# Kernel tuning notes

Measured on AMD Instinct MI355X. Metric: run time of the kernel, lower is better.

The kernel has to match this reference:

```python
import jax, jax.numpy as jnp
import numpy as np

SIGMA = 0.05
SIGMA2 = SIGMA * SIGMA
N_NODES = 100000
N_EDGES = 3200000


def setup_inputs() -> dict:
    key = jax.random.key(0)
    k1, k2, k3, k4 = jax.random.split(key, 4)
    source_points = jax.random.normal(k1, (N_NODES, 3), dtype=jnp.float32)
    target_points = jax.random.normal(k2, (N_NODES, 3), dtype=jnp.float32)
    edge_index = jax.random.randint(k3, (2, N_EDGES), 0, N_NODES, dtype=jnp.int64)
    edge_weights = jax.random.uniform(k4, (N_EDGES, 1), dtype=jnp.float32)
    return {"source_points": source_points, "target_points": target_points,
            "edge_index": edge_index, "edge_weights": edge_weights}


def reference(source_points, target_points, edge_index, edge_weights):
    N = source_points.shape[0]
    dst = edge_index[0]  # center point each edge contributes to
    nbr = edge_index[1]  # neighbor point index

    src_nb = source_points[nbr]            # [E,3]
    tgt_nb = target_points[nbr]            # [E,3]

    ones_e = jnp.ones((edge_index.shape[1],), dtype=source_points.dtype)
    counts = jnp.maximum(jax.ops.segment_sum(ones_e, dst, num_segments=N), 1.0)[:, None]
    src_centers = jax.ops.segment_sum(src_nb, dst, num_segments=N) / counts  # [N,3]
    tgt_centers = jax.ops.segment_sum(tgt_nb, dst, num_segments=N) / counts  # [N,3]

    src_diff = (src_nb - src_centers[dst]) * edge_weights  # [E,3]
    tgt_diff = tgt_nb - tgt_centers[dst]                   # [E,3]

    # per-edge outer product, scattered to per-point 3x3 covariances
    edge_mats = src_diff[:, :, None] * tgt_diff[:, None, :]          # [E,3,3]
    point_mats = jax.ops.segment_sum(edge_mats, dst, num_segments=N)  # [N,3,3]

    U, S, Vh = jnp.linalg.svd(point_mats)  # torch.svd's V = Vh^T, so U @ V^T == U @ Vh
    R0 = jnp.matmul(U, Vh)
    det = jnp.linalg.det(R0)
    ones_n = jnp.ones((N,), dtype=source_points.dtype)
    d_diag = jax.lax.stop_gradient(jnp.stack([ones_n, ones_n, det], axis=-1))  # [N,3]
    R = jnp.matmul(U * d_diag[:, None, :], Vh)  # U @ diag(d) @ Vh, proper rotation

    trans = tgt_centers - jnp.einsum('nij,nj->ni', R, src_centers)  # [N,3]

    # apply each neighbor's rigid transform and compute robust weights
    transformed = jnp.einsum('eij,ej->ei', R[nbr], src_nb) + trans[nbr]  # [E,3]
    d2 = jnp.sum(jnp.square(transformed - tgt_nb), axis=-1, keepdims=True)  # [E,1]
    new_edge_weights = SIGMA2 / (d2 + SIGMA2)
    return (R, trans, new_edge_weights)
```

## Files before the change

### kernel.cpp

```cpp
#include <hip/hip_runtime.h>
#include <math.h>

static constexpr float kSigma2 = 0.05f * 0.05f;
static constexpr int kCap = 6400;

__device__ __forceinline__ int load_idx(const void* ei, long long j, int is64) {
    if (is64) return (int)(((const long long*)ei)[j]);
    return ((const int*)ei)[j];
}

__global__ void k_detect(const int* __restrict__ ei32, int E, int* __restrict__ nz) {
    int t = threadIdx.x;
    int lim = E < 2048 ? E : 2048;
    int acc = 0;
    for (int k = t; k < lim; k += blockDim.x) acc |= ei32[2 * k + 1];
    if (acc) atomicOr(nz, 1);
}

__global__ void k_pack(const float* __restrict__ src, const float* __restrict__ tgt,
                       float4* __restrict__ s4, float4* __restrict__ t4, int N) {
    int i = blockIdx.x * blockDim.x + threadIdx.x;
    if (i >= N) return;
    s4[i] = make_float4(src[3 * i + 0], src[3 * i + 1], src[3 * i + 2], 0.0f);
    t4[i] = make_float4(tgt[3 * i + 0], tgt[3 * i + 1], tgt[3 * i + 2], 0.0f);
}

__device__ void kabsch_from_M(const double M[3][3], double Rm[3][3]) {
    Rm[0][0] = 1; Rm[0][1] = 0; Rm[0][2] = 0;
    Rm[1][0] = 0; Rm[1][1] = 1; Rm[1][2] = 0;
    Rm[2][0] = 0; Rm[2][1] = 0; Rm[2][2] = 1;

    double frob2 = 0.0;
#pragma unroll
    for (int r = 0; r < 3; ++r)
#pragma unroll
        for (int c = 0; c < 3; ++c) frob2 += M[r][c] * M[r][c];
    if (frob2 <= 1e-80) return;

    double A[3][3];
#pragma unroll
    for (int r = 0; r < 3; ++r)
#pragma unroll
        for (int c = 0; c < 3; ++c) {
            double s = 0.0;
#pragma unroll
            for (int k = 0; k < 3; ++k) s += M[k][r] * M[k][c];
            A[r][c] = s;
        }
    double V[3][3] = {{1, 0, 0}, {0, 1, 0}, {0, 0, 1}};
    const int PL[3] = {0, 0, 1};
    const int QL[3] = {1, 2, 2};
    for (int sweep = 0; sweep < 15; ++sweep) {
        double off = fabs(A[0][1]) + fabs(A[0][2]) + fabs(A[1][2]);
        if (off == 0.0) break;
        for (int pi = 0; pi < 3; ++pi) {
            int p = PL[pi], q = QL[pi], r3 = 3 - p - q;
            double apq = A[p][q];
            if (apq == 0.0) continue;
            double theta = (A[q][q] - A[p][p]) / (2.0 * apq);
            double t = copysign(1.0, theta) / (fabs(theta) + sqrt(theta * theta + 1.0));
            double c = 1.0 / sqrt(t * t + 1.0);
            double s = t * c;
            A[p][p] -= t * apq;
            A[q][q] += t * apq;
            A[p][q] = 0.0; A[q][p] = 0.0;
            double arp = A[r3][p], arq = A[r3][q];
            A[r3][p] = c * arp - s * arq; A[p][r3] = A[r3][p];
            A[r3][q] = s * arp + c * arq; A[q][r3] = A[r3][q];
#pragma unroll
            for (int k = 0; k < 3; ++k) {
                double vp = V[k][p], vq = V[k][q];
                V[k][p] = c * vp - s * vq;
                V[k][q] = s * vp + c * vq;
            }
        }
    }
    double lam[3] = {A[0][0], A[1][1], A[2][2]};
    int id0 = 0, id1 = 1, id2 = 2, tt;
    if (lam[id0] < lam[id1]) { tt = id0; id0 = id1; id1 = tt; }
    if (lam[id0] < lam[id2]) { tt = id0; id0 = id2; id2 = tt; }
    if (lam[id1] < lam[id2]) { tt = id1; id1 = id2; id2 = tt; }
    double v1[3] = {V[0][id0], V[1][id0], V[2][id0]};
    double v2[3] = {V[0][id1], V[1][id1], V[2][id1]};
    double v3[3] = {V[0][id2], V[1][id2], V[2][id2]};

    double b1[3], b2[3];
#pragma unroll
    for (int r = 0; r < 3; ++r) {
        b1[r] = M[r][0] * v1[0] + M[r][1] * v1[1] + M[r][2] * v1[2];
        b2[r] = M[r][0] * v2[0] + M[r][1] * v2[1] + M[r][2] * v2[2];
    }
    double n1 = sqrt(b1[0] * b1[0] + b1[1] * b1[1] + b1[2] * b1[2]);
    if (n1 <= 1e-150) return;
    double u1[3] = {b1[0] / n1, b1[1] / n1, b1[2] / n1};
    double dot = u1[0] * b2[0] + u1[1] * b2[1] + u1[2] * b2[2];
    double w2[3] = {b2[0] - dot * u1[0], b2[1] - dot * u1[1], b2[2] - dot * u1[2]};
    double n2 = sqrt(w2[0] * w2[0] + w2[1] * w2[1] + w2[2] * w2[2]);
    double u2[3];
    if (n2 > n1 * 1e-12) {
        u2[0] = w2[0] / n2; u2[1] = w2[1] / n2; u2[2] = w2[2] / n2;
    } else {
        double ex0 = (fabs(u1[0]) < 0.9) ? 1.0 : 0.0;
        double ex1 = 1.0 - ex0;
        double cx = u1[1] * 0.0 - u1[2] * ex1;
        double cy = u1[2] * ex0 - u1[0] * 0.0;
        double cz = u1[0] * ex1 - u1[1] * ex0;
        double cn = sqrt(cx * cx + cy * cy + cz * cz);
        u2[0] = cx / cn; u2[1] = cy / cn; u2[2] = cz / cn;
    }
    double u3[3] = {u1[1] * u2[2] - u1[2] * u2[1],
                    u1[2] * u2[0] - u1[0] * u2[2],
                    u1[0] * u2[1] - u1[1] * u2[0]};
    double dV = v1[0] * (v2[1] * v3[2] - v2[2] * v3[1])
              - v1[1] * (v2[0] * v3[2] - v2[2] * v3[0])
              + v1[2] * (v2[0] * v3[1] - v2[1] * v3[0]);
    dV = (dV >= 0.0) ? 1.0 : -1.0;
#pragma unroll
    for (int r = 0; r < 3; ++r)
#pragma unroll
        for (int c = 0; c < 3; ++c)
            Rm[r][c] = u1[r] * v1[c] + u2[r] * v2[c] + dV * u3[r] * v3[c];
}


__global__ void __launch_bounds__(256) k_bhist(const void* __restrict__ ei,
                                               int* __restrict__ btot16,
                                               const int* __restrict__ nz,
                                               int E, int N, int nbuckets) {
    __shared__ int lhist[1024];
    int t = threadIdx.x;
    long long tile = (long long)blockIdx.x * 16384;
    long long remll = (long long)E - tile;
    int rem = (remll < 16384) ? (int)remll : 16384;
    int is64 = (*nz == 0);
    for (int i = t; i < 1024; i += 256) lhist[i] = 0;
    __syncthreads();
    if (rem == 16384) {
        for (int it = 0; it < 8; ++it) {
            long long base = tile + (long long)it * 2048 + (long long)t * 8;
            int d[8];
            if (is64) {
                const long long* p = (const long long*)ei + base;
#pragma unroll
                for (int k = 0; k < 4; ++k) {
                    longlong2 v = ((const longlong2*)p)[k];
                    d[2 * k] = (int)v.x;
                    d[2 * k + 1] = (int)v.y;
                }
            } else {
                const int* p = (const int*)ei + base;
                int4 a = ((const int4*)p)[0];
                int4 bb = ((const int4*)p)[1];
                d[0] = a.x; d[1] = a.y; d[2] = a.z; d[3] = a.w;
                d[4] = bb.x; d[5] = bb.y; d[6] = bb.z; d[7] = bb.w;
            }
#pragma unroll
            for (int k = 0; k < 8; ++k)
                if ((unsigned)d[k] < (unsigned)N) atomicAdd(&lhist[d[k] >> 7], 1);
        }
    } else {
        for (int idx = t; idx < rem; idx += 256) {
            int d = load_idx(ei, tile + idx, is64);
            if ((unsigned)d < (unsigned)N) atomicAdd(&lhist[d >> 7], 1);
        }
    }
    __syncthreads();
    for (int b = t; b < 1024; b += 256) {
        int c = lhist[b];
        if (c > 0 && b < nbuckets) atomicAdd(&btot16[b * 16], c);
    }
}

__global__ void k_scan(const int* __restrict__ btot16, int* __restrict__ boff,
                       int* __restrict__ cur16, int* __restrict__ curC16, int nbuckets) {
    __shared__ int sm[1024];
    int t = threadIdx.x;
    int v = (t < nbuckets) ? btot16[t * 16] : 0;
    sm[t] = v;
    __syncthreads();
    for (int s = 1; s < 1024; s <<= 1) {
        int x = (t >= s) ? sm[t - s] : 0;
        __syncthreads();
        sm[t] += x;
        __syncthreads();
    }
    if (t < nbuckets) {
        int excl = sm[t] - v;
        boff[t] = excl;
        cur16[t * 16] = excl;
        if ((t & 63) == 0) curC16[(t >> 6) * 16] = excl;
    }
    if (t == nbuckets - 1) boff[nbuckets] = sm[t];
}

__global__ void __launch_bounds__(256) k_cscatter(const void* __restrict__ ei,
                                                  const float* __restrict__ ew,
                                                  int* __restrict__ curC16,
                                                  int2* __restrict__ sedge1,
                                                  const int* __restrict__ nz,
                                                  int E, int N, int ncoarse) {
    __shared__ int2 stage[2048];
    __shared__ unsigned char binOf[2048];
    __shared__ int hist[16];
    __shared__ int excl[16];
    __shared__ int gbase[16];
    int t = threadIdx.x;
    long long tile = (long long)blockIdx.x * 2048;
    long long remll = (long long)E - tile;
    int rem = (remll < 2048) ? (int)remll : 2048;
    int is64 = (*nz == 0);
    if (t < 16) hist[t] = 0;
    __syncthreads();

    int dd[8], nn[8];
    float ww[8];
    int cnt8 = 0;
    if (rem == 2048) {
        if (is64) {
            const long long* pd = (const long long*)ei + tile + (long long)t * 8;
            const long long* pn = (const long long*)ei + (long long)E + tile + (long long)t * 8;
#pragma unroll
            for (int k = 0; k < 4; ++k) {
                longlong2 vd = ((const longlong2*)pd)[k];
                longlong2 vn = ((const longlong2*)pn)[k];
                dd[2 * k] = (int)vd.x; dd[2 * k + 1] = (int)vd.y;
                nn[2 * k] = (int)vn.x; nn[2 * k + 1] = (int)vn.y;
            }
        } else {
            const int* pd = (const int*)ei + tile + (long long)t * 8;
            const int* pn = (const int*)ei + (long long)E + tile + (long long)t * 8;
            int4 a = ((const int4*)pd)[0], b = ((const int4*)pd)[1];
            int4 c = ((const int4*)pn)[0], d = ((const int4*)pn)[1];
            dd[0] = a.x; dd[1] = a.y; dd[2] = a.z; dd[3] = a.w;
            dd[4] = b.x; dd[5] = b.y; dd[6] = b.z; dd[7] = b.w;
            nn[0] = c.x; nn[1] = c.y; nn[2] = c.z; nn[3] = c.w;
            nn[4] = d.x; nn[5] = d.y; nn[6] = d.z; nn[7] = d.w;
        }
        const float* pw = ew + tile + (long long)t * 8;
        float4 wa = ((const float4*)pw)[0], wb = ((const float4*)pw)[1];
        ww[0] = wa.x; ww[1] = wa.y; ww[2] = wa.z; ww[3] = wa.w;
        ww[4] = wb.x; ww[5] = wb.y; ww[6] = wb.z; ww[7] = wb.w;
        cnt8 = 8;
    } else {
        int base = t * 8;
#pragma unroll
        for (int k = 0; k < 8; ++k) {
            int idx = base + k;
            if (idx < rem) {
                long long e = tile + idx;
                dd[cnt8] = load_idx(ei, e, is64);
                nn[cnt8] = load_idx(ei, (long long)E + e, is64);
                ww[cnt8] = ew[e];
                ++cnt8;
            }
        }
    }

    int mybin[8], myrank[8];
    int2 mypay[8];
#pragma unroll
    for (int k = 0; k < 8; ++k) {
        mybin[k] = -1;
        if (k < cnt8) {
            int d = dd[k];
            if ((unsigned)d < (unsigned)N) {
                int n = nn[k];
                if ((unsigned)n >= (unsigned)N) n = N;
                int cb = d >> 13;
                mybin[k] = cb;
                myrank[k] = atomicAdd(&hist[cb], 1);
                mypay[k].x = (n << 13) | (d & 8191);
                mypay[k].y = __float_as_int(ww[k]);
            }
        }
    }
    __syncthreads();
    if (t == 0) {
        int run = 0;
#pragma unroll
        for (int c = 0; c < 16; ++c) { excl[c] = run; run += hist[c]; }
    }
    __syncthreads();
#pragma unroll
    for (int k = 0; k < 8; ++k) {
        if (mybin[k] >= 0) {
            int lpos = excl[mybin[k]] + myrank[k];
            stage[lpos] = mypay[k];
            binOf[lpos] = (unsigned char)mybin[k];
        }
    }
    if (t < 16) {
        int c = hist[t];
        gbase[t] = (c > 0 && t < ncoarse) ? atomicAdd(&curC16[t * 16], c) : 0;
    }
    __syncthreads();
    int total = excl[15] + hist[15];
    for (int lpos = t; lpos < total; lpos += 256) {
        int c = binOf[lpos];
        sedge1[gbase[c] + (lpos - excl[c])] = stage[lpos];
    }
}

__global__ void __launch_bounds__(256) k_fscatter(const int2* __restrict__ sedge1,
                                                  int* __restrict__ cur16,
                                                  const int* __restrict__ boff,
                                                  int2* __restrict__ sedge2,
                                                  int E, int nbuckets, int ncoarse) {
    __shared__ int2 stage[2048];
    __shared__ unsigned short binOf[2048];
    __shared__ int lhist[1024];
    __shared__ int lincl[1024];
    __shared__ int gbase[1024];
    __shared__ int co[17];
    __shared__ int s_clo, s_W;
    int t = threadIdx.x;
    if (t <= ncoarse) {
        int f = t * 64;
        if (f > nbuckets) f = nbuckets;
        co[t] = boff[f];
    }
    __syncthreads();
    int Ev = co[ncoarse];
    long long tile = (long long)blockIdx.x * 2048;
    if (tile >= Ev) return;
    long long remll = (long long)Ev - tile;
    int rem = (remll < 2048) ? (int)remll : 2048;

    if (t == 0) {
        long long p0 = tile, p1 = tile + rem - 1;
        int c0 = 0;
        while (c0 + 1 < ncoarse && p0 >= co[c0 + 1]) ++c0;
        int c1 = c0;
        while (c1 + 1 < ncoarse && p1 >= co[c1 + 1]) ++c1;
        s_clo = c0;
        s_W = (c1 - c0 + 1) * 64;
    }
    __syncthreads();
    int clo = s_clo, W = s_W;
    for (int i = t; i < W; i += 256) lhist[i] = 0;
    __syncthreads();

    int2 pay[8];
    int cnt8 = 0;
    if (rem == 2048) {
        const int4* p4 = (const int4*)(sedge1 + tile + (long long)t * 8);
#pragma unroll
        for (int k = 0; k < 4; ++k) {
            int4 v = p4[k];
            pay[2 * k].x = v.x; pay[2 * k].y = v.y;
            pay[2 * k + 1].x = v.z; pay[2 * k + 1].y = v.w;
        }
        cnt8 = 8;
    } else {
        int base = t * 8;
#pragma unroll
        for (int k = 0; k < 8; ++k) {
            int idx = base + k;
            if (idx < rem) pay[cnt8++] = sedge1[tile + idx];
        }
    }

    int mybin[8], myrank[8];
    int2 mypay[8];
#pragma unroll
    for (int k = 0; k < 8; ++k) {
        mybin[k] = -1;
        if (k < cnt8) {
            long long pos = tile + t * 8 + k;
            int c = clo;
            while (c + 1 < ncoarse && pos >= co[c + 1]) ++c;
            int x1 = pay[k].x;
            unsigned nbr = ((unsigned)x1) >> 13;
            int rel = (c - clo) * 64 + ((x1 & 8191) >> 7);
            mybin[k] = rel;
            myrank[k] = atomicAdd(&lhist[rel], 1);
            mypay[k].x = (int)((nbr << 7) | (unsigned)(x1 & 127));
            mypay[k].y = pay[k].y;
        }
    }
    __syncthreads();
    for (int i = t; i < W; i += 256) lincl[i] = lhist[i];
    __syncthreads();
    for (int s = 1; s < W; s <<= 1) {
        int tmp[4];
        int cj = 0;
        for (int i = t; i < W; i += 256) tmp[cj++] = (i >= s) ? lincl[i - s] : 0;
        __syncthreads();
        cj = 0;
        for (int i = t; i < W; i += 256) lincl[i] += tmp[cj++];
        __syncthreads();
    }
#pragma unroll
    for (int k = 0; k < 8; ++k) {
        if (mybin[k] >= 0) {
            int ex = lincl[mybin[k]] - lhist[mybin[k]];
            int lpos = ex + myrank[k];
            stage[lpos] = mypay[k];
            binOf[lpos] = (unsigned short)mybin[k];
        }
    }
    __syncthreads();
    for (int rel = t; rel < W; rel += 256) {
        int c = lhist[rel];
        int fin = clo * 64 + rel;
        gbase[rel] = (c > 0 && fin < nbuckets) ? atomicAdd(&cur16[fin * 16], c) : 0;
    }
    __syncthreads();
    int total = lincl[W - 1];
    for (int lpos = t; lpos < total; lpos += 256) {
        int rel = binOf[lpos];
        int ex = lincl[rel] - lhist[rel];
        sedge2[gbase[rel] + (lpos - ex)] = stage[lpos];
    }
}

__global__ void __launch_bounds__(256) k_binscatter(const void* __restrict__ ei,
                                                    const float* __restrict__ ew,
                                                    int* __restrict__ cur16,
                                                    int2* __restrict__ sedge,
                                                    const int* __restrict__ nz,
                                                    int E, int N, int nbuckets) {
    __shared__ int2 stage[2048];
    __shared__ unsigned short binOf[2048];
    __shared__ int lhist[1024];
    __shared__ int lincl[1024];
    __shared__ int gbase[1024];
    int t = threadIdx.x;
    long long tile = (long long)blockIdx.x * 2048;
    long long remll = (long long)E - tile;
    int rem = (remll < 2048) ? (int)remll : 2048;
    int is64 = (*nz == 0);
    for (int i = t; i < 1024; i += 256) lhist[i] = 0;
    __syncthreads();

    int dd[8], nn[8];
    float ww[8];
    int cnt8 = 0;
    if (rem == 2048) {
        if (is64) {
            const long long* pd = (const long long*)ei + tile + (long long)t * 8;
            const long long* pn = (const long long*)ei + (long long)E + tile + (long long)t * 8;
#pragma unroll
            for (int k = 0; k < 4; ++k) {
                longlong2 vd = ((const longlong2*)pd)[k];
                longlong2 vn = ((const longlong2*)pn)[k];
                dd[2 * k] = (int)vd.x; dd[2 * k + 1] = (int)vd.y;
                nn[2 * k] = (int)vn.x; nn[2 * k + 1] = (int)vn.y;
            }
        } else {
            const int* pd = (const int*)ei + tile + (long long)t * 8;
            const int* pn = (const int*)ei + (long long)E + tile + (long long)t * 8;
            int4 a = ((const int4*)pd)[0], b = ((const int4*)pd)[1];
            int4 c = ((const int4*)pn)[0], d = ((const int4*)pn)[1];
            dd[0] = a.x; dd[1] = a.y; dd[2] = a.z; dd[3] = a.w;
            dd[4] = b.x; dd[5] = b.y; dd[6] = b.z; dd[7] = b.w;
            nn[0] = c.x; nn[1] = c.y; nn[2] = c.z; nn[3] = c.w;
            nn[4] = d.x; nn[5] = d.y; nn[6] = d.z; nn[7] = d.w;
        }
        const float* pw = ew + tile + (long long)t * 8;
        float4 wa = ((const float4*)pw)[0], wb = ((const float4*)pw)[1];
        ww[0] = wa.x; ww[1] = wa.y; ww[2] = wa.z; ww[3] = wa.w;
        ww[4] = wb.x; ww[5] = wb.y; ww[6] = wb.z; ww[7] = wb.w;
        cnt8 = 8;
    } else {
        int base = t * 8;
#pragma unroll
        for (int k = 0; k < 8; ++k) {
            int idx = base + k;
            if (idx < rem) {
                long long e = tile + idx;
                dd[cnt8] = load_idx(ei, e, is64);
                nn[cnt8] = load_idx(ei, (long long)E + e, is64);
                ww[cnt8] = ew[e];
                ++cnt8;
            }
        }
    }

    int mybin[8];
    int myrank[8];
    int2 mypay[8];
#pragma unroll
    for (int k = 0; k < 8; ++k) {
        mybin[k] = -1;
        if (k < cnt8) {
            int d = dd[k];
            if ((unsigned)d < (unsigned)N) {
                int n = nn[k];
                if ((unsigned)n >= (unsigned)N) n = N;
                int bb = d >> 7;
                mybin[k] = bb;
                myrank[k] = atomicAdd(&lhist[bb], 1);
                mypay[k].x = (n << 7) | (d & 127);
                mypay[k].y = __float_as_int(ww[k]);
            }
        }
    }
    __syncthreads();
    for (int i = t; i < 1024; i += 256) lincl[i] = lhist[i];
    __syncthreads();
    for (int s = 1; s < 1024; s <<= 1) {
        int tmp[4];
#pragma unroll
        for (int j = 0; j < 4; ++j) {
            int i = (j << 8) + t;
            tmp[j] = (i >= s) ? lincl[i - s] : 0;
        }
        __syncthreads();
#pragma unroll
        for (int j = 0; j < 4; ++j) {
            int i = (j << 8) + t;
            lincl[i] += tmp[j];
        }
        __syncthreads();
    }
#pragma unroll
    for (int k = 0; k < 8; ++k) {
        if (mybin[k] >= 0) {
            int ex = lincl[mybin[k]] - lhist[mybin[k]];
            int lpos = ex + myrank[k];
            stage[lpos] = mypay[k];
            binOf[lpos] = (unsigned short)mybin[k];
        }
    }
    __syncthreads();
    for (int bb = t; bb < 1024; bb += 256) {
        int c = lhist[bb];
        gbase[bb] = (c > 0 && bb < nbuckets) ? atomicAdd(&cur16[bb * 16], c) : 0;
    }
    __syncthreads();
    int total = lincl[1023];
    for (int lpos = t; lpos < total; lpos += 256) {
        int bb = binOf[lpos];
        int ex = lincl[bb] - lhist[bb];
        sedge[gbase[bb] + (lpos - ex)] = stage[lpos];
    }
}

__global__ void __launch_bounds__(256) k_sort(const int* __restrict__ boff,
                                              int2* __restrict__ sedge,
                                              int2* __restrict__ nseg) {
    __shared__ int2 sorted[kCap];
    __shared__ int hist[128];
    __shared__ int scanbuf[128];
    __shared__ int offs[128];
    __shared__ int cur[128];
    int b = blockIdx.x, t = threadIdx.x;
    int e0 = boff[b], e1 = boff[b + 1];
    int cnt = e1 - e0;
    if (t < 128) hist[t] = 0;
    __syncthreads();
    if (cnt <= kCap) {
        for (int i = t; i < cnt; i += 256)
            atomicAdd(&hist[sedge[e0 + i].x & 127], 1);
        __syncthreads();
        if (t < 128) scanbuf[t] = hist[t];
        __syncthreads();
        for (int s = 1; s < 128; s <<= 1) {
            int v = 0;
            if (t < 128 && t >= s) v = scanbuf[t - s];
            __syncthreads();
            if (t < 128) scanbuf[t] += v;
            __syncthreads();
        }
        if (t < 128) {
            int ex = scanbuf[t] - hist[t];
            offs[t] = ex;
            cur[t] = ex;
        }
        __syncthreads();
        for (int i = t; i < cnt; i += 256) {
            int2 p = sedge[e0 + i];
            int r = atomicAdd(&cur[p.x & 127], 1);
            sorted[r] = p;
        }
        __syncthreads();
        for (int i = t; i < cnt; i += 256) sedge[e0 + i] = sorted[i];
        if (t < 128) nseg[b * 128 + t] = make_int2(e0 + offs[t], hist[t]);
    } else {
        if (t < 128) nseg[b * 128 + t] = make_int2(e0, -cnt);
    }
}

__global__ void __launch_bounds__(256) k_moment(const int2* __restrict__ nseg,
                                                const int2* __restrict__ sedge,
                                                const float4* __restrict__ s4,
                                                const float4* __restrict__ t4,
                                                float* __restrict__ momG, int N) {
    int b = blockIdx.x, t = threadIdx.x;
    int oct = t >> 3, lane8 = t & 7;
    int base = b * 64;
    for (int node = base + oct; node < base + 64; node += 32) {
        if (node >= N) break;
        int2 seg = nseg[node];
        float v[23];
#pragma unroll
        for (int i = 0; i < 23; ++i) v[i] = 0.0f;
        int start = seg.x;
        int cn = seg.y;
        int total = (cn >= 0) ? cn : -cn;
        int filter = (cn < 0);
        int nlow = node & 127;
        for (int j = lane8; j < total; j += 8) {
            int2 p = sedge[start + j];
            if (filter && (p.x & 127) != nlow) continue;
            unsigned n = ((unsigned)p.x) >> 7;
            if (n >= (unsigned)N) continue;
            float w = __int_as_float(p.y);
            float4 a = s4[n];
            float4 bb = t4[n];
            float sx = a.x, sy = a.y, sz = a.z;
            float tx = bb.x, ty = bb.y, tz = bb.z;
            v[0] += 1.0f;
            v[1] += sx; v[2] += sy; v[3] += sz;
            v[4] += tx; v[5] += ty; v[6] += tz;
            v[7] += w;
            float wsx = w * sx, wsy = w * sy, wsz = w * sz;
            v[8] += wsx; v[9] += wsy; v[10] += wsz;
            v[11] += w * tx; v[12] += w * ty; v[13] += w * tz;
            v[14] += wsx * tx; v[15] += wsx * ty; v[16] += wsx * tz;
            v[17] += wsy * tx; v[18] += wsy * ty; v[19] += wsy * tz;
            v[20] += wsz * tx; v[21] += wsz * ty; v[22] += wsz * tz;
        }
#pragma unroll
        for (int m = 1; m < 8; m <<= 1) {
#pragma unroll
            for (int i = 0; i < 23; ++i) v[i] += __shfl_xor(v[i], m, 64);
        }
        if (lane8 == 0) {
#pragma unroll
            for (int i = 0; i < 23; ++i) momG[(size_t)i * N + node] = v[i];
        }
    }
}

__global__ void __launch_bounds__(256) k_kabsch2(const float* __restrict__ momG,
                                                 const float4* __restrict__ s4,
                                                 const float4* __restrict__ t4,
                                                 float* __restrict__ Rout,
                                                 float* __restrict__ Tout,
                                                 float* __restrict__ wnode, int N) {
    int i = blockIdx.x * blockDim.x + threadIdx.x;
    if (i >= N) return;
    float m[23];
#pragma unroll
    for (int k = 0; k < 23; ++k) m[k] = momG[(size_t)k * N + i];
    double cntv = (double)m[0];
    double inv = 1.0 / fmax(cntv, 1.0);
    double sb[3] = {m[1] * inv, m[2] * inv, m[3] * inv};
    double tb[3] = {m[4] * inv, m[5] * inv, m[6] * inv};
    double Sw = m[7];
    double Sws[3] = {m[8], m[9], m[10]};
    double Swt[3] = {m[11], m[12], m[13]};
    double M[3][3];
#pragma unroll
    for (int r = 0; r < 3; ++r)
#pragma unroll
        for (int c = 0; c < 3; ++c)
            M[r][c] = (double)m[14 + 3 * r + c]
                    - sb[r] * Swt[c] - Sws[r] * tb[c] + Sw * sb[r] * tb[c];
    double Rm[3][3];
    kabsch_from_M(M, Rm);
    double T0 = tb[0] - (Rm[0][0] * sb[0] + Rm[0][1] * sb[1] + Rm[0][2] * sb[2]);
    double T1 = tb[1] - (Rm[1][0] * sb[0] + Rm[1][1] * sb[1] + Rm[1][2] * sb[2]);
    double T2 = tb[2] - (Rm[2][0] * sb[0] + Rm[2][1] * sb[1] + Rm[2][2] * sb[2]);
#pragma unroll
    for (int r = 0; r < 3; ++r)
#pragma unroll
        for (int c = 0; c < 3; ++c)
            Rout[9 * (long long)i + 3 * r + c] = (float)Rm[r][c];
    Tout[3 * i + 0] = (float)T0;
    Tout[3 * i + 1] = (float)T1;
    Tout[3 * i + 2] = (float)T2;
    float4 a = s4[i];
    float4 q = t4[i];
    double x0 = Rm[0][0] * a.x + Rm[0][1] * a.y + Rm[0][2] * a.z + T0;
    double x1 = Rm[1][0] * a.x + Rm[1][1] * a.y + Rm[1][2] * a.z + T1;
    double x2 = Rm[2][0] * a.x + Rm[2][1] * a.y + Rm[2][2] * a.z + T2;
    double d0 = x0 - q.x, d1 = x1 - q.y, d2 = x2 - q.z;
    double dd = d0 * d0 + d1 * d1 + d2 * d2;
    wnode[i] = (float)((double)kSigma2 / (dd + (double)kSigma2));
}

__global__ void __launch_bounds__(256) k_wgather(const void* __restrict__ ei,
                                                 const float* __restrict__ wnode,
                                                 float* __restrict__ wout,
                                                 const int* __restrict__ nz,
                                                 int E, int N) {
    int gid = blockIdx.x * blockDim.x + threadIdx.x;
    long long base = (long long)gid * 8;
    if (base >= E) return;
    int is64 = (*nz == 0);
    int n_[8];
    int full = (base + 8 <= (long long)E);
    if (full) {
        if (is64) {
            const long long* p = (const long long*)ei + (long long)E + base;
#pragma unroll
            for (int k = 0; k < 4; ++k) {
                longlong2 a = ((const longlong2*)p)[k];
                n_[2 * k] = (int)a.x;
                n_[2 * k + 1] = (int)a.y;
            }
        } else {
            const int* p = (const int*)ei + (long long)E + base;
            int4 a = ((const int4*)p)[0];
            int4 b = ((const int4*)p)[1];
            n_[0] = a.x; n_[1] = a.y; n_[2] = a.z; n_[3] = a.w;
            n_[4] = b.x; n_[5] = b.y; n_[6] = b.z; n_[7] = b.w;
        }
        float w[8];
#pragma unroll
        for (int k = 0; k < 8; ++k)
            w[k] = ((unsigned)n_[k] < (unsigned)N) ? wnode[n_[k]] : 1.0f;
        *(float4*)(wout + base) = make_float4(w[0], w[1], w[2], w[3]);
        *(float4*)(wout + base + 4) = make_float4(w[4], w[5], w[6], w[7]);
    } else {
#pragma unroll
        for (int k = 0; k < 8; ++k) {
            long long e = base + k;
            if (e < E) {
                int n = load_idx(ei, (long long)E + e, is64);
                wout[e] = ((unsigned)n < (unsigned)N) ? wnode[n] : 1.0f;
            }
        }
    }
}


__global__ void k_accum1(const void* __restrict__ ei, const float* __restrict__ src,
                         const float* __restrict__ tgt, float* __restrict__ cnt,
                         float* __restrict__ ssum, float* __restrict__ tsum,
                         const int* __restrict__ nz, int E, int N) {
    int e = blockIdx.x * blockDim.x + threadIdx.x;
    if (e >= E) return;
    int is64 = (*nz == 0);
    int d = load_idx(ei, e, is64);
    int n = load_idx(ei, (long long)E + e, is64);
    if ((unsigned)d >= (unsigned)N || (unsigned)n >= (unsigned)N) return;
    atomicAdd(&cnt[d], 1.0f);
    atomicAdd(&ssum[3 * d + 0], src[3 * n + 0]);
    atomicAdd(&ssum[3 * d + 1], src[3 * n + 1]);
    atomicAdd(&ssum[3 * d + 2], src[3 * n + 2]);
    atomicAdd(&tsum[3 * d + 0], tgt[3 * n + 0]);
    atomicAdd(&tsum[3 * d + 1], tgt[3 * n + 1]);
    atomicAdd(&tsum[3 * d + 2], tgt[3 * n + 2]);
}

__global__ void k_centers(float* __restrict__ cnt, float* __restrict__ ssum,
                          float* __restrict__ tsum, int N) {
    int i = blockIdx.x * blockDim.x + threadIdx.x;
    if (i >= N) return;
    float inv = 1.0f / fmaxf(cnt[i], 1.0f);
    ssum[3 * i + 0] *= inv; ssum[3 * i + 1] *= inv; ssum[3 * i + 2] *= inv;
    tsum[3 * i + 0] *= inv; tsum[3 * i + 1] *= inv; tsum[3 * i + 2] *= inv;
}

__global__ void k_accum2(const void* __restrict__ ei, const float* __restrict__ src,
                         const float* __restrict__ tgt, const float* __restrict__ ew,
                         const float* __restrict__ sc, const float* __restrict__ tc,
                         float* __restrict__ Mm, const int* __restrict__ nz, int E, int N) {
    int e = blockIdx.x * blockDim.x + threadIdx.x;
    if (e >= E) return;
    int is64 = (*nz == 0);
    int d = load_idx(ei, e, is64);
    int n = load_idx(ei, (long long)E + e, is64);
    if ((unsigned)d >= (unsigned)N || (unsigned)n >= (unsigned)N) return;
    float w = ew[e];
    float a0 = (src[3 * n + 0] - sc[3 * d + 0]) * w;
    float a1 = (src[3 * n + 1] - sc[3 * d + 1]) * w;
    float a2 = (src[3 * n + 2] - sc[3 * d + 2]) * w;
    float b0 = tgt[3 * n + 0] - tc[3 * d + 0];
    float b1 = tgt[3 * n + 1] - tc[3 * d + 1];
    float b2 = tgt[3 * n + 2] - tc[3 * d + 2];
    float* Md = Mm + 9 * (long long)d;
    atomicAdd(Md + 0, a0 * b0); atomicAdd(Md + 1, a0 * b1); atomicAdd(Md + 2, a0 * b2);
    atomicAdd(Md + 3, a1 * b0); atomicAdd(Md + 4, a1 * b1); atomicAdd(Md + 5, a1 * b2);
    atomicAdd(Md + 6, a2 * b0); atomicAdd(Md + 7, a2 * b1); atomicAdd(Md + 8, a2 * b2);
}

__global__ void k_kabsch(const float* __restrict__ Mm, const float* __restrict__ sc,
                         const float* __restrict__ tc, float* __restrict__ Rout,
                         float* __restrict__ Tout, int N) {
    int i = blockIdx.x * blockDim.x + threadIdx.x;
    if (i >= N) return;
    double M[3][3];
#pragma unroll
    for (int r = 0; r < 3; ++r)
#pragma unroll
        for (int c = 0; c < 3; ++c)
            M[r][c] = (double)Mm[9 * (long long)i + 3 * r + c];
    double Rm[3][3];
    kabsch_from_M(M, Rm);
    double s0 = sc[3 * i + 0], s1 = sc[3 * i + 1], s2 = sc[3 * i + 2];
    double t0 = tc[3 * i + 0], t1 = tc[3 * i + 1], t2 = tc[3 * i + 2];
#pragma unroll
    for (int r = 0; r < 3; ++r)
#pragma unroll
        for (int c = 0; c < 3; ++c)
            Rout[9 * (long long)i + 3 * r + c] = (float)Rm[r][c];
    Tout[3 * i + 0] = (float)(t0 - (Rm[0][0] * s0 + Rm[0][1] * s1 + Rm[0][2] * s2));
    Tout[3 * i + 1] = (float)(t1 - (Rm[1][0] * s0 + Rm[1][1] * s1 + Rm[1][2] * s2));
    Tout[3 * i + 2] = (float)(t2 - (Rm[2][0] * s0 + Rm[2][1] * s1 + Rm[2][2] * s2));
}

__global__ void k_weights_plain(const void* __restrict__ ei,
                                const float* __restrict__ src,
                                const float* __restrict__ tgt,
                                const float* __restrict__ R,
                                const float* __restrict__ T,
                                float* __restrict__ wout,
                                const int* __restrict__ nz, int E, int N) {
    int e = blockIdx.x * blockDim.x + threadIdx.x;
    if (e >= E) return;
    int is64 = (*nz == 0);
    int n = load_idx(ei, (long long)E + e, is64);
    float w = 1.0f;
    if ((unsigned)n < (unsigned)N) {
        float p0 = src[3 * n + 0], p1 = src[3 * n + 1], p2 = src[3 * n + 2];
        float q0 = tgt[3 * n + 0], q1 = tgt[3 * n + 1], q2 = tgt[3 * n + 2];
        const float* Rn = R + 9 * (long long)n;
        const float* Tn = T + 3 * (long long)n;
        float x0 = Rn[0] * p0 + Rn[1] * p1 + Rn[2] * p2 + Tn[0];
        float x1 = Rn[3] * p0 + Rn[4] * p1 + Rn[5] * p2 + Tn[1];
        float x2 = Rn[6] * p0 + Rn[7] * p1 + Rn[8] * p2 + Tn[2];
        float d0 = x0 - q0, d1 = x1 - q1, d2 = x2 - q2;
        float dd = d0 * d0 + d1 * d1 + d2 * d2;
        w = kSigma2 / (dd + kSigma2);
    }
    wout[e] = w;
}

extern "C" void kernel_launch(void* const* d_in, const int* in_sizes, int n_in,
                              void* d_out, int out_size, void* d_ws, size_t ws_size,
                              hipStream_t stream) {
    const float* src = (const float*)d_in[0];
    const float* tgt = (const float*)d_in[1];
    const void* ei = d_in[2];
    const float* ew = (const float*)d_in[3];
    int N = in_sizes[0] / 3;
    int E = in_sizes[3];

    float* out = (float*)d_out;
    float* Rout = out;
    float* Tout = out + (size_t)9 * N;
    float* Wout = out + (size_t)12 * N;

    int eb = (E + 255) / 256;
    int nb = (N + 255) / 256;
    int nb64 = (N + 63) / 64;
    int nbuckets = (N + 127) / 128;
    int ncoarse = (nbuckets + 63) / 64;
    int tiles = (int)(((long long)E + 2047) / 2048);
    int tiles16 = (int)(((long long)E + 16383) / 16384);
    int wb8 = (int)(((long long)E + 2047) / 2048);

    size_t ctrl_ints = 16 + (size_t)nbuckets * 16 * 2 + 256 + (nbuckets + 1);
    ctrl_ints = (ctrl_ints + 3) & ~(size_t)3;
    size_t after1 = ctrl_ints + 2 * (size_t)E;
    after1 = (after1 + 3) & ~(size_t)3;
    size_t after2 = after1 + 2 * (size_t)E;
    after2 = (after2 + 3) & ~(size_t)3;
    size_t tail_ints = 8 * (size_t)N + (size_t)N + 23 * (size_t)N
                     + 2 * (size_t)128 * nbuckets;
    size_t needA = (after2 + tail_ints) * sizeof(int);
    size_t needB = (after1 + tail_ints) * sizeof(int);

    if (N <= 131072 && nbuckets <= 1024 && ws_size >= needB) {
        int twolevel = (ws_size >= needA) ? 1 : 0;
        int* nz = (int*)d_ws;
        int* btot16 = nz + 16;
        int* cur16 = btot16 + (size_t)nbuckets * 16;
        int* curC16 = cur16 + (size_t)nbuckets * 16;
        int* boff = curC16 + 256;
        int2* sedge1 = (int2*)((int*)d_ws + ctrl_ints);
        size_t tail_base = twolevel ? after2 : after1;
        int2* sedge2 = twolevel ? (int2*)((int*)d_ws + after1) : sedge1;
        float4* s4 = (float4*)((int*)d_ws + tail_base);
        float4* t4 = s4 + N;
        float* wnode = (float*)(t4 + N);
        float* momG = wnode + N;
        int2* nseg = (int2*)(momG + 23 * (size_t)N);

        hipMemsetAsync(d_ws, 0, ctrl_ints * sizeof(int), stream);

        k_detect<<<1, 256, 0, stream>>>((const int*)ei, E, nz);
        k_pack<<<nb, 256, 0, stream>>>(src, tgt, s4, t4, N);
        k_bhist<<<tiles16, 256, 0, stream>>>(ei, btot16, nz, E, N, nbuckets);
        k_scan<<<1, 1024, 0, stream>>>(btot16, boff, cur16, curC16, nbuckets);
        if (twolevel) {
            k_cscatter<<<tiles, 256, 0, stream>>>(ei, ew, curC16, sedge1, nz, E, N, ncoarse);
            k_fscatter<<<tiles, 256, 0, stream>>>(sedge1, cur16, boff, sedge2, E, nbuckets, ncoarse);
        } else {
            k_binscatter<<<tiles, 256, 0, stream>>>(ei, ew, cur16, sedge2, nz, E, N, nbuckets);
        }
        k_sort<<<nbuckets, 256, 0, stream>>>(boff, sedge2, nseg);
        k_moment<<<nb64, 256, 0, stream>>>(nseg, sedge2, s4, t4, momG, N);
        k_kabsch2<<<nb, 256, 0, stream>>>(momG, s4, t4, Rout, Tout, wnode, N);
        k_wgather<<<wb8, 256, 0, stream>>>(ei, wnode, Wout, nz, E, N);
    } else {
        float* cnt = (float*)d_ws;
        float* ssum = cnt + N;
        float* tsum = ssum + 3 * (size_t)N;
        float* Mm = tsum + 3 * (size_t)N;
        int* nz = (int*)(Mm + 9 * (size_t)N);
        size_t ws_bytes = (size_t)16 * N * sizeof(float) + 16;
        hipMemsetAsync(d_ws, 0, ws_bytes, stream);
        k_detect<<<1, 256, 0, stream>>>((const int*)ei, E, nz);
        k_accum1<<<eb, 256, 0, stream>>>(ei, src, tgt, cnt, ssum, tsum, nz, E, N);
        k_centers<<<nb, 256, 0, stream>>>(cnt, ssum, tsum, N);
        k_accum2<<<eb, 256, 0, stream>>>(ei, src, tgt, ew, ssum, tsum, Mm, nz, E, N);
        k_kabsch<<<nb, 256, 0, stream>>>(Mm, ssum, tsum, Rout, Tout, N);
        k_weights_plain<<<eb, 256, 0, stream>>>(ei, src, tgt, Rout, Tout, Wout, nz, E, N);
    }
}
```

Baseline: 272.1 us.

## Fuse per-bucket sort with moment accumulation using 64-node buckets

```diff
diff --git a/kernel.cpp b/kernel.cpp
--- a/kernel.cpp
+++ b/kernel.cpp
@@ -2,7 +2,7 @@
 #include <math.h>
 
 static constexpr float kSigma2 = 0.05f * 0.05f;
-static constexpr int kCap = 6400;
+static constexpr int kCap2 = 2560;
 
 __device__ __forceinline__ int load_idx(const void* ei, long long j, int is64) {
     if (is64) return (int)(((const long long*)ei)[j]);
@@ -127,13 +127,13 @@
                                                int* __restrict__ btot16,
                                                const int* __restrict__ nz,
                                                int E, int N, int nbuckets) {
-    __shared__ int lhist[1024];
+    __shared__ int lhist[2048];
     int t = threadIdx.x;
     long long tile = (long long)blockIdx.x * 16384;
     long long remll = (long long)E - tile;
     int rem = (remll < 16384) ? (int)remll : 16384;
     int is64 = (*nz == 0);
-    for (int i = t; i < 1024; i += 256) lhist[i] = 0;
+    for (int i = t; i < 2048; i += 256) lhist[i] = 0;
     __syncthreads();
     if (rem == 16384) {
         for (int it = 0; it < 8; ++it) {
@@ -156,16 +156,16 @@
             }
 #pragma unroll
             for (int k = 0; k < 8; ++k)
-                if ((unsigned)d[k] < (unsigned)N) atomicAdd(&lhist[d[k] >> 7], 1);
+                if ((unsigned)d[k] < (unsigned)N) atomicAdd(&lhist[d[k] >> 6], 1);
         }
     } else {
         for (int idx = t; idx < rem; idx += 256) {
             int d = load_idx(ei, tile + idx, is64);
-            if ((unsigned)d < (unsigned)N) atomicAdd(&lhist[d >> 7], 1);
-        }
-    }
-    __syncthreads();
-    for (int b = t; b < 1024; b += 256) {
+            if ((unsigned)d < (unsigned)N) atomicAdd(&lhist[d >> 6], 1);
+        }
+    }
+    __syncthreads();
+    for (int b = t; b < 2048; b += 256) {
         int c = lhist[b];
         if (c > 0 && b < nbuckets) atomicAdd(&btot16[b * 16], c);
     }
@@ -173,24 +173,36 @@
 
 __global__ void k_scan(const int* __restrict__ btot16, int* __restrict__ boff,
                        int* __restrict__ cur16, int* __restrict__ curC16, int nbuckets) {
-    __shared__ int sm[1024];
+    __shared__ int sm[2048];
     int t = threadIdx.x;
-    int v = (t < nbuckets) ? btot16[t * 16] : 0;
-    sm[t] = v;
-    __syncthreads();
-    for (int s = 1; s < 1024; s <<= 1) {
-        int x = (t >= s) ? sm[t - s] : 0;
+    int v0 = (t < nbuckets) ? btot16[t * 16] : 0;
+    int v1 = (t + 1024 < nbuckets) ? btot16[(t + 1024) * 16] : 0;
+    sm[t] = v0;
+    sm[t + 1024] = v1;
+    __syncthreads();
+    for (int s = 1; s < 2048; s <<= 1) {
+        int x0 = (t >= s) ? sm[t - s] : 0;
+        int x1 = (t + 1024 >= s) ? sm[t + 1024 - s] : 0;
         __syncthreads();
-        sm[t] += x;
+        sm[t] += x0;
+        sm[t + 1024] += x1;
         __syncthreads();
     }
     if (t < nbuckets) {
-        int excl = sm[t] - v;
-        boff[t] = excl;
-        cur16[t * 16] = excl;
-        if ((t & 63) == 0) curC16[(t >> 6) * 16] = excl;
+        int ex = sm[t] - v0;
+        boff[t] = ex;
+        cur16[t * 16] = ex;
+        if ((t & 127) == 0) curC16[(t >> 7) * 16] = ex;
+    }
+    int t2 = t + 1024;
+    if (t2 < nbuckets) {
+        int ex = sm[t2] - v1;
+        boff[t2] = ex;
+        cur16[t2 * 16] = ex;
+        if ((t2 & 127) == 0) curC16[(t2 >> 7) * 16] = ex;
     }
     if (t == nbuckets - 1) boff[nbuckets] = sm[t];
+    if (t2 == nbuckets - 1) boff[nbuckets] = sm[t2];
 }
 
 __global__ void __launch_bounds__(256) k_cscatter(const void* __restrict__ ei,
@@ -315,7 +327,7 @@
     __shared__ int s_clo, s_W;
     int t = threadIdx.x;
     if (t <= ncoarse) {
-        int f = t * 64;
+        int f = t * 128;
         if (f > nbuckets) f = nbuckets;
         co[t] = boff[f];
     }
@@ -333,12 +345,10 @@
         int c1 = c0;
         while (c1 + 1 < ncoarse && p1 >= co[c1 + 1]) ++c1;
         s_clo = c0;
-        s_W = (c1 - c0 + 1) * 64;
+        s_W = (c1 - c0 + 1) * 128;
     }
     __syncthreads();
     int clo = s_clo, W = s_W;
-    for (int i = t; i < W; i += 256) lhist[i] = 0;
-    __syncthreads();
 
     int2 pay[8];
     int cnt8 = 0;
@@ -359,6 +369,26 @@
             if (idx < rem) pay[cnt8++] = sedge1[tile + idx];
         }
     }
+
+    if (W > 1024) {
+        for (int k = 0; k < cnt8; ++k) {
+            long long pos = tile + t * 8 + k;
+            int c = clo;
+            while (c + 1 < ncoarse && pos >= co[c + 1]) ++c;
+            int x1 = pay[k].x;
+            unsigned nbr = ((unsigned)x1) >> 13;
+            int fin = c * 128 + ((x1 & 8191) >> 6);
+            int gpos = atomicAdd(&cur16[fin * 16], 1);
+            int2 out;
+            out.x = (int)((nbr << 6) | (unsigned)(x1 & 63));
+            out.y = pay[k].y;
+            sedge2[gpos] = out;
+        }
+        return;
+    }
+
+    for (int i = t; i < W; i += 256) lhist[i] = 0;
+    __syncthreads();
 
     int mybin[8], myrank[8];
     int2 mypay[8];
@@ -371,10 +401,10 @@
             while (c + 1 < ncoarse && pos >= co[c + 1]) ++c;
             int x1 = pay[k].x;
             unsigned nbr = ((unsigned)x1) >> 13;
-            int rel = (c - clo) * 64 + ((x1 & 8191) >> 7);
+            int rel = (c - clo) * 128 + ((x1 & 8191) >> 6);
             mybin[k] = rel;
             myrank[k] = atomicAdd(&lhist[rel], 1);
-            mypay[k].x = (int)((nbr << 7) | (unsigned)(x1 & 127));
+            mypay[k].x = (int)((nbr << 6) | (unsigned)(x1 & 63));
             mypay[k].y = pay[k].y;
         }
     }
@@ -402,7 +432,7 @@
     __syncthreads();
     for (int rel = t; rel < W; rel += 256) {
         int c = lhist[rel];
-        int fin = clo * 64 + rel;
+        int fin = clo * 128 + rel;
         gbase[rel] = (c > 0 && fin < nbuckets) ? atomicAdd(&cur16[fin * 16], c) : 0;
     }
     __syncthreads();
@@ -422,15 +452,15 @@
                                                     int E, int N, int nbuckets) {
     __shared__ int2 stage[2048];
     __shared__ unsigned short binOf[2048];
-    __shared__ int lhist[1024];
-    __shared__ int lincl[1024];
-    __shared__ int gbase[1024];
+    __shared__ int lhist[2048];
+    __shared__ int lincl[2048];
+    __shared__ int gbase[2048];
     int t = threadIdx.x;
     long long tile = (long long)blockIdx.x * 2048;
     long long remll = (long long)E - tile;
     int rem = (remll < 2048) ? (int)remll : 2048;
     int is64 = (*nz == 0);
-    for (int i = t; i < 1024; i += 256) lhist[i] = 0;
+    for (int i = t; i < 2048; i += 256) lhist[i] = 0;
     __syncthreads();
 
     int dd[8], nn[8];
@@ -488,27 +518,27 @@
             if ((unsigned)d < (unsigned)N) {
                 int n = nn[k];
                 if ((unsigned)n >= (unsigned)N) n = N;
-                int bb = d >> 7;
+                int bb = d >> 6;
                 mybin[k] = bb;
                 myrank[k] = atomicAdd(&lhist[bb], 1);
-                mypay[k].x = (n << 7) | (d & 127);
+                mypay[k].x = (n << 6) | (d & 63);
                 mypay[k].y = __float_as_int(ww[k]);
             }
         }
     }
     __syncthreads();
-    for (int i = t; i < 1024; i += 256) lincl[i] = lhist[i];
-    __syncthreads();
-    for (int s = 1; s < 1024; s <<= 1) {
-        int tmp[4];
-#pragma unroll
-        for (int j = 0; j < 4; ++j) {
+    for (int i = t; i < 2048; i += 256) lincl[i] = lhist[i];
+    __syncthreads();
+    for (int s = 1; s < 2048; s <<= 1) {
+        int tmp[8];
+#pragma unroll
+        for (int j = 0; j < 8; ++j) {
             int i = (j << 8) + t;
             tmp[j] = (i >= s) ? lincl[i - s] : 0;
         }
         __syncthreads();
 #pragma unroll
-        for (int j = 0; j < 4; ++j) {
+        for (int j = 0; j < 8; ++j) {
             int i = (j << 8) + t;
             lincl[i] += tmp[j];
         }
@@ -524,12 +554,12 @@
         }
     }
     __syncthreads();
-    for (int bb = t; bb < 1024; bb += 256) {
+    for (int bb = t; bb < 2048; bb += 256) {
         int c = lhist[bb];
         gbase[bb] = (c > 0 && bb < nbuckets) ? atomicAdd(&cur16[bb * 16], c) : 0;
     }
     __syncthreads();
-    int total = lincl[1023];
+    int total = lincl[2047];
     for (int lpos = t; lpos < total; lpos += 256) {
         int bb = binOf[lpos];
         int ex = lincl[bb] - lhist[bb];
@@ -537,97 +567,110 @@
     }
 }
 
-__global__ void __launch_bounds__(256) k_sort(const int* __restrict__ boff,
-                                              int2* __restrict__ sedge,
-                                              int2* __restrict__ nseg) {
-    __shared__ int2 sorted[kCap];
-    __shared__ int hist[128];
-    __shared__ int scanbuf[128];
-    __shared__ int offs[128];
-    __shared__ int cur[128];
+__global__ void __launch_bounds__(256) k_sortmoment(const int* __restrict__ boff,
+                                                    const int2* __restrict__ sedge2,
+                                                    const float4* __restrict__ s4,
+                                                    const float4* __restrict__ t4,
+                                                    float* __restrict__ momG, int N) {
+    __shared__ int2 sorted[kCap2];
+    __shared__ int hist[64];
+    __shared__ int scanbuf[64];
+    __shared__ int offs[64];
+    __shared__ int cur[64];
     int b = blockIdx.x, t = threadIdx.x;
     int e0 = boff[b], e1 = boff[b + 1];
     int cnt = e1 - e0;
-    if (t < 128) hist[t] = 0;
-    __syncthreads();
-    if (cnt <= kCap) {
+    if (t < 64) hist[t] = 0;
+    __syncthreads();
+    int inlds = (cnt <= kCap2);
+    if (inlds) {
         for (int i = t; i < cnt; i += 256)
-            atomicAdd(&hist[sedge[e0 + i].x & 127], 1);
+            atomicAdd(&hist[sedge2[e0 + i].x & 63], 1);
         __syncthreads();
-        if (t < 128) scanbuf[t] = hist[t];
+        if (t < 64) scanbuf[t] = hist[t];
         __syncthreads();
-        for (int s = 1; s < 128; s <<= 1) {
+        for (int s = 1; s < 64; s <<= 1) {
             int v = 0;
-            if (t < 128 && t >= s) v = scanbuf[t - s];
+            if (t < 64 && t >= s) v = scanbuf[t - s];
             __syncthreads();
-            if (t < 128) scanbuf[t] += v;
+            if (t < 64) scanbuf[t] += v;
             __syncthreads();
         }
-        if (t < 128) {
+        if (t < 64) {
             int ex = scanbuf[t] - hist[t];
             offs[t] = ex;
             cur[t] = ex;
         }
         __syncthreads();
         for (int i = t; i < cnt; i += 256) {
-            int2 p = sedge[e0 + i];
-            int r = atomicAdd(&cur[p.x & 127], 1);
+            int2 p = sedge2[e0 + i];
+            int r = atomicAdd(&cur[p.x & 63], 1);
             sorted[r] = p;
         }
         __syncthreads();
-        for (int i = t; i < cnt; i += 256) sedge[e0 + i] = sorted[i];
-        if (t < 128) nseg[b * 128 + t] = make_int2(e0 + offs[t], hist[t]);
-    } else {
-        if (t < 128) nseg[b * 128 + t] = make_int2(e0, -cnt);
-    }
-}
-
-__global__ void __launch_bounds__(256) k_moment(const int2* __restrict__ nseg,
-                                                const int2* __restrict__ sedge,
-                                                const float4* __restrict__ s4,
-                                                const float4* __restrict__ t4,
-                                                float* __restrict__ momG, int N) {
-    int b = blockIdx.x, t = threadIdx.x;
+    }
     int oct = t >> 3, lane8 = t & 7;
-    int base = b * 64;
-    for (int node = base + oct; node < base + 64; node += 32) {
-        if (node >= N) break;
-        int2 seg = nseg[node];
+#pragma unroll
+    for (int rr = 0; rr < 2; ++rr) {
+        int nl = oct + rr * 32;
+        long long node = (long long)b * 64 + nl;
         float v[23];
 #pragma unroll
         for (int i = 0; i < 23; ++i) v[i] = 0.0f;
-        int start = seg.x;
-        int cn = seg.y;
-        int total = (cn >= 0) ? cn : -cn;
-        int filter = (cn < 0);
-        int nlow = node & 127;
-        for (int j = lane8; j < total; j += 8) {
-            int2 p = sedge[start + j];
-            if (filter && (p.x & 127) != nlow) continue;
-            unsigned n = ((unsigned)p.x) >> 7;
-            if (n >= (unsigned)N) continue;
-            float w = __int_as_float(p.y);
-            float4 a = s4[n];
-            float4 bb = t4[n];
-            float sx = a.x, sy = a.y, sz = a.z;
-            float tx = bb.x, ty = bb.y, tz = bb.z;
-            v[0] += 1.0f;
-            v[1] += sx; v[2] += sy; v[3] += sz;
-            v[4] += tx; v[5] += ty; v[6] += tz;
-            v[7] += w;
-            float wsx = w * sx, wsy = w * sy, wsz = w * sz;
-            v[8] += wsx; v[9] += wsy; v[10] += wsz;
-            v[11] += w * tx; v[12] += w * ty; v[13] += w * tz;
-            v[14] += wsx * tx; v[15] += wsx * ty; v[16] += wsx * tz;
-            v[17] += wsy * tx; v[18] += wsy * ty; v[19] += wsy * tz;
-            v[20] += wsz * tx; v[21] += wsz * ty; v[22] += wsz * tz;
+        if (node < N) {
+            if (inlds) {
+                int start = offs[nl];
+                int cn = hist[nl];
+                for (int j = lane8; j < cn; j += 8) {
+                    int2 p = sorted[start + j];
+                    unsigned n = ((unsigned)p.x) >> 6;
+                    if (n >= (unsigned)N) continue;
+                    float w = __int_as_float(p.y);
+                    float4 a = s4[n];
+                    float4 bb = t4[n];
+                    float sx = a.x, sy = a.y, sz = a.z;
+                    float tx = bb.x, ty = bb.y, tz = bb.z;
+                    v[0] += 1.0f;
+                    v[1] += sx; v[2] += sy; v[3] += sz;
+                    v[4] += tx; v[5] += ty; v[6] += tz;
+                    v[7] += w;
+                    float wsx = w * sx, wsy = w * sy, wsz = w * sz;
+                    v[8] += wsx; v[9] += wsy; v[10] += wsz;
+                    v[11] += w * tx; v[12] += w * ty; v[13] += w * tz;
+                    v[14] += wsx * tx; v[15] += wsx * ty; v[16] += wsx * tz;
+                    v[17] += wsy * tx; v[18] += wsy * ty; v[19] += wsy * tz;
+                    v[20] += wsz * tx; v[21] += wsz * ty; v[22] += wsz * tz;
+                }
+            } else {
+                for (int j = lane8; j < cnt; j += 8) {
+                    int2 p = sedge2[e0 + j];
+                    if ((p.x & 63) != nl) continue;
+                    unsigned n = ((unsigned)p.x) >> 6;
+                    if (n >= (unsigned)N) continue;
+                    float w = __int_as_float(p.y);
+                    float4 a = s4[n];
+                    float4 bb = t4[n];
+                    float sx = a.x, sy = a.y, sz = a.z;
+                    float tx = bb.x, ty = bb.y, tz = bb.z;
+                    v[0] += 1.0f;
+                    v[1] += sx; v[2] += sy; v[3] += sz;
+                    v[4] += tx; v[5] += ty; v[6] += tz;
+                    v[7] += w;
+                    float wsx = w * sx, wsy = w * sy, wsz = w * sz;
+                    v[8] += wsx; v[9] += wsy; v[10] += wsz;
+                    v[11] += w * tx; v[12] += w * ty; v[13] += w * tz;
+                    v[14] += wsx * tx; v[15] += wsx * ty; v[16] += wsx * tz;
+                    v[17] += wsy * tx; v[18] += wsy * ty; v[19] += wsy * tz;
+                    v[20] += wsz * tx; v[21] += wsz * ty; v[22] += wsz * tz;
+                }
+            }
         }
 #pragma unroll
         for (int m = 1; m < 8; m <<= 1) {
 #pragma unroll
             for (int i = 0; i < 23; ++i) v[i] += __shfl_xor(v[i], m, 64);
         }
-        if (lane8 == 0) {
+        if (lane8 == 0 && node < N) {
 #pragma unroll
             for (int i = 0; i < 23; ++i) momG[(size_t)i * N + node] = v[i];
         }
@@ -848,9 +891,8 @@
 
     int eb = (E + 255) / 256;
     int nb = (N + 255) / 256;
-    int nb64 = (N + 63) / 64;
-    int nbuckets = (N + 127) / 128;
-    int ncoarse = (nbuckets + 63) / 64;
+    int nbuckets = (N + 63) / 64;
+    int ncoarse = (nbuckets + 127) / 128;
     int tiles = (int)(((long long)E + 2047) / 2048);
     int tiles16 = (int)(((long long)E + 16383) / 16384);
     int wb8 = (int)(((long long)E + 2047) / 2048);
@@ -861,12 +903,11 @@
     after1 = (after1 + 3) & ~(size_t)3;
     size_t after2 = after1 + 2 * (size_t)E;
     after2 = (after2 + 3) & ~(size_t)3;
-    size_t tail_ints = 8 * (size_t)N + (size_t)N + 23 * (size_t)N
-                     + 2 * (size_t)128 * nbuckets;
+    size_t tail_ints = 8 * (size_t)N + (size_t)N + 23 * (size_t)N;
     size_t needA = (after2 + tail_ints) * sizeof(int);
     size_t needB = (after1 + tail_ints) * sizeof(int);
 
-    if (N <= 131072 && nbuckets <= 1024 && ws_size >= needB) {
+    if (N <= 131072 && nbuckets <= 2048 && ws_size >= needB) {
         int twolevel = (ws_size >= needA) ? 1 : 0;
         int* nz = (int*)d_ws;
         int* btot16 = nz + 16;
@@ -880,7 +921,6 @@
         float4* t4 = s4 + N;
         float* wnode = (float*)(t4 + N);
         float* momG = wnode + N;
-        int2* nseg = (int2*)(momG + 23 * (size_t)N);
 
         hipMemsetAsync(d_ws, 0, ctrl_ints * sizeof(int), stream);
 
@@ -894,8 +934,7 @@
         } else {
             k_binscatter<<<tiles, 256, 0, stream>>>(ei, ew, cur16, sedge2, nz, E, N, nbuckets);
         }
-        k_sort<<<nbuckets, 256, 0, stream>>>(boff, sedge2, nseg);
-        k_moment<<<nb64, 256, 0, stream>>>(nseg, sedge2, s4, t4, momG, N);
+        k_sortmoment<<<nbuckets, 256, 0, stream>>>(boff, sedge2, s4, t4, momG, N);
         k_kabsch2<<<nb, 256, 0, stream>>>(momG, s4, t4, Rout, Tout, wnode, N);
         k_wgather<<<wb8, 256, 0, stream>>>(ei, wnode, Wout, nz, E, N);
     } else {
```

After: 262.0 us. 3.7% less time.
